# Kernel optimization log

Measured on AMD Instinct MI355X. Metric: run time of the kernel, lower is better.

The kernel has to match this reference:

```python
import jax, jax.numpy as jnp
import numpy as np


def silu(x):
    return x * jax.nn.sigmoid(x)


def setup_inputs() -> dict:
    key = jax.random.key(0)
    ks = jax.random.split(key, 12)
    B, S, Dm = 2, 2048, 768
    I, N, R, K = 1536, 16, 48, 4
    s = 0.02
    return {
        "input_states": jax.random.normal(ks[0], (B, S, Dm), jnp.float32),
        "in_proj_w": jax.random.normal(ks[1], (2 * I, Dm), jnp.float32) * s,
        "conv_w": jax.random.normal(ks[2], (I, 1, K), jnp.float32) * s,
        "conv_b": jax.random.normal(ks[3], (I,), jnp.float32) * s,
        "x_proj_w": jax.random.normal(ks[4], (R + 2 * N, I), jnp.float32) * s,
        "dt_proj_w": jax.random.normal(ks[5], (I, R), jnp.float32) * s,
        "dt_proj_b": jax.random.normal(ks[6], (I,), jnp.float32) * s,
        "A_log": jax.random.normal(ks[7], (I, N), jnp.float32) * 0.5,
        "D": jax.random.normal(ks[8], (I,), jnp.float32) * s,
        "out_proj_w": jax.random.normal(ks[9], (Dm, I), jnp.float32) * s,
        "alpha": jax.random.uniform(ks[10], (I,), jnp.float32),
        "feature_gating": jax.random.uniform(ks[11], (I,), jnp.float32),
    }


def reference(input_states, in_proj_w, conv_w, conv_b, x_proj_w,
              dt_proj_w, dt_proj_b, A_log, D, out_proj_w,
              alpha, feature_gating):
    Bsz, S, _ = input_states.shape
    I, N = A_log.shape
    R = dt_proj_w.shape[1]
    K = conv_w.shape[-1]

    # in_proj (no bias), chunk into hidden / gate, each [B, I, S]
    proj = jnp.einsum('bsd,ed->bse', input_states, in_proj_w)  # [B, S, 2I]
    hidden, gate = jnp.split(proj.transpose(0, 2, 1), 2, axis=1)

    # causal depthwise conv1d + SiLU
    h = jax.lax.conv_general_dilated(
        hidden, conv_w, window_strides=(1,), padding=[(K - 1, 0)],
        dimension_numbers=('NCH', 'OIH', 'NCH'), feature_group_count=I)
    h = silu(h + conv_b[None, :, None])  # [B, I, S]

    # x_proj -> time_step, B, C
    ssm_p = jnp.einsum('bis,ei->bse', h, x_proj_w)  # [B, S, R+2N]
    ts, Bm, Cm = jnp.split(ssm_p, [R, R + N], axis=-1)

    dt = jax.nn.softplus(jnp.einsum('bsr,ir->bsi', ts, dt_proj_w) + dt_proj_b)
    dt = dt.transpose(0, 2, 1)                       # [B, I, S]
    dt = dt.at[:, :, -1].multiply(alpha[None, :])    # alpha scales last step

    A = -jnp.exp(A_log.astype(jnp.float32))          # [I, N]
    dA = jnp.exp(A[None, :, None, :] * dt[:, :, :, None])       # [B, I, S, N]
    dBu = dt[:, :, :, None] * Bm[:, None, :, :] * h[:, :, :, None]  # [B, I, S, N]

    def step(state, xs):
        dA_t, dBu_t, C_t = xs
        state = dA_t * state + dBu_t                 # [B, I, N]
        y = jnp.einsum('bin,bn->bi', state, C_t)
        return state, y

    init = jnp.zeros((Bsz, I, N), input_states.dtype)
    _, ys = jax.lax.scan(
        step, init,
        (dA.transpose(2, 0, 1, 3), dBu.transpose(2, 0, 1, 3), Cm.transpose(1, 0, 2)))
    y = ys.transpose(1, 2, 0)                        # [B, I, S]

    y = (y + h * D[None, :, None]) * silu(gate)
    y = y.at[:, :, -1].multiply(feature_gating[None, :])
    return jnp.einsum('bis,di->bsd', y, out_proj_w)  # [B, S, Dm]
```

## Files before the change

### kernel.cpp

```cpp
#include <hip/hip_runtime.h>
#include <math.h>


static constexpr int S_LEN  = 2048;
static constexpr int DMODEL = 768;
static constexpr int ICH    = 1536;
static constexpr int NST    = 16;
static constexpr int MROWS  = 4096;
static constexpr int NCH    = 64;
static constexpr int CHS    = 32;
static constexpr int CSTR   = 2 * ICH * NST;

typedef _Float16 f16;
typedef f16 f16x8 __attribute__((ext_vector_type(8)));
typedef f16 f16x4 __attribute__((ext_vector_type(4)));
typedef f16 f16x2 __attribute__((ext_vector_type(2)));
typedef float f32x4 __attribute__((ext_vector_type(4)));

typedef __attribute__((address_space(3))) void lds_void;
typedef const __attribute__((address_space(1))) void glb_void;

__device__ __forceinline__ void glds16(f16* l, const f16* g) {
    __builtin_amdgcn_global_load_lds((glb_void*)g, (lds_void*)l, 16, 0, 0);
}

__device__ __forceinline__ float silu_f(float x) {
    return x / (1.0f + __expf(-x));
}

__global__ __launch_bounds__(256) void cvt3(
    const float* __restrict__ s0, f16* __restrict__ d0, int n0,
    const float* __restrict__ s1, f16* __restrict__ d1, int n1,
    const float* __restrict__ s2, f16* __restrict__ d2)
{
    int i = (blockIdx.x * 256 + threadIdx.x) * 4;
    const float* s; f16* d;
    if (i < n0)            { s = s0 + i;            d = d0 + i; }
    else if (i < n0 + n1)  { s = s1 + (i - n0);     d = d1 + (i - n0); }
    else                   { s = s2 + (i - n0 - n1); d = d2 + (i - n0 - n1); }
    float4 v = *(const float4*)s;
    f16x4 o = { (f16)v.x, (f16)v.y, (f16)v.z, (f16)v.w };
    *(f16x4*)d = o;
}

__global__ __launch_bounds__(256) void k1m(
    const f16* __restrict__ Xh,
    const f16* __restrict__ Wh,
    f16* __restrict__ hidden,
    f16* __restrict__ sgate)
{
    __shared__ __align__(16) f16 As[2][128 * 32];
    __shared__ __align__(16) f16 Bs[2][128 * 32];
    const int tid = threadIdx.x;
    const int lane = tid & 63, wave = tid >> 6;
    const int quad = lane >> 4, l16 = lane & 15;
    const int wm = wave & 1, wn = wave >> 1;
    const int m0 = blockIdx.x * 128, n0 = blockIdx.y * 128;
    const int l_row = lane >> 2, l_c8 = (lane & 3) * 8;

    const f16* Ag = Xh + (size_t)(m0 + wave * 16 + l_row) * 768 + l_c8;
    const f16* Bg = Wh + (size_t)(n0 + wave * 16 + l_row) * 768 + l_c8;
    const int lo = (wave * 16) * 32, hi = (64 + wave * 16) * 32;

    f32x4 acc[4][4] = {};
    for (int k0 = 0; k0 < 768; k0 += 64) {
        __syncthreads();
        glds16(&As[0][lo], Ag + k0);
        glds16(&As[0][hi], Ag + (size_t)64 * 768 + k0);
        glds16(&Bs[0][lo], Bg + k0);
        glds16(&Bs[0][hi], Bg + (size_t)64 * 768 + k0);
        glds16(&As[1][lo], Ag + k0 + 32);
        glds16(&As[1][hi], Ag + (size_t)64 * 768 + k0 + 32);
        glds16(&Bs[1][lo], Bg + k0 + 32);
        glds16(&Bs[1][hi], Bg + (size_t)64 * 768 + k0 + 32);
        __syncthreads();
        #pragma unroll
        for (int half = 0; half < 2; ++half) {
            f16x8 af[4], bf[4];
            #pragma unroll
            for (int mi = 0; mi < 4; ++mi)
                af[mi] = *(const f16x8*)&As[half][(wm * 64 + mi * 16 + l16) * 32 + quad * 8];
            #pragma unroll
            for (int ni = 0; ni < 4; ++ni)
                bf[ni] = *(const f16x8*)&Bs[half][(wn * 64 + ni * 16 + l16) * 32 + quad * 8];
            #pragma unroll
            for (int mi = 0; mi < 4; ++mi)
                #pragma unroll
                for (int ni = 0; ni < 4; ++ni)
                    acc[mi][ni] = __builtin_amdgcn_mfma_f32_16x16x32_f16(
                        af[mi], bf[ni], acc[mi][ni], 0, 0, 0);
        }
    }
    const bool isGate = (n0 >= ICH);
    f16* outp = isGate ? sgate : hidden;
    const int e0 = (isGate ? (n0 - ICH) : n0) + wn * 64 + l16;
    #pragma unroll
    for (int mi = 0; mi < 4; ++mi) {
        #pragma unroll
        for (int ni = 0; ni < 4; ++ni) {
            #pragma unroll
            for (int r = 0; r < 4; ++r) {
                int m = m0 + wm * 64 + mi * 16 + quad * 4 + r;
                int e = e0 + ni * 16;
                float v = acc[mi][ni][r];
                if (isGate) v = silu_f(v);
                outp[(size_t)m * ICH + e] = (f16)v;
            }
        }
    }
}

__global__ __launch_bounds__(256) void k2_conv(
    const f16* __restrict__ hidden,
    const float* __restrict__ conv_w,
    const float* __restrict__ conv_b,
    f16* __restrict__ h)
{
    int idx = blockIdx.x * 256 + threadIdx.x;
    int i4 = idx % 384;
    int m  = idx / 384;
    int s  = m & (S_LEN - 1);
    const f16* base = hidden + (size_t)m * ICH + i4 * 4;
    const int c0 = i4 * 4;
    float4 wa = *(const float4*)(conv_w + (c0 + 0) * 4);
    float4 wb = *(const float4*)(conv_w + (c0 + 1) * 4);
    float4 wc = *(const float4*)(conv_w + (c0 + 2) * 4);
    float4 wd = *(const float4*)(conv_w + (c0 + 3) * 4);
    float4 bv = *(const float4*)(conv_b + c0);
    f16x4 z = {};
    f16x4 x0 = *(const f16x4*)(base);
    f16x4 x1 = (s >= 1) ? *(const f16x4*)(base - ICH)     : z;
    f16x4 x2 = (s >= 2) ? *(const f16x4*)(base - 2 * ICH) : z;
    f16x4 x3 = (s >= 3) ? *(const f16x4*)(base - 3 * ICH) : z;
    float r0 = bv.x + wa.x * (float)x3[0] + wa.y * (float)x2[0] + wa.z * (float)x1[0] + wa.w * (float)x0[0];
    float r1 = bv.y + wb.x * (float)x3[1] + wb.y * (float)x2[1] + wb.z * (float)x1[1] + wb.w * (float)x0[1];
    float r2 = bv.z + wc.x * (float)x3[2] + wc.y * (float)x2[2] + wc.z * (float)x1[2] + wc.w * (float)x0[2];
    float r3 = bv.w + wd.x * (float)x3[3] + wd.y * (float)x2[3] + wd.z * (float)x1[3] + wd.w * (float)x0[3];
    f16x4 r = { (f16)silu_f(r0), (f16)silu_f(r1), (f16)silu_f(r2), (f16)silu_f(r3) };
    *(f16x4*)(h + (size_t)m * ICH + i4 * 4) = r;
}

__global__ __launch_bounds__(256) void k3_xproj(
    const f16* __restrict__ h,
    const float* __restrict__ xw,
    float* __restrict__ ssmp)
{
    __shared__ float4 As[64][5];
    __shared__ float4 Bs[80][5];
    const int tid = threadIdx.x;
    const int tm = tid >> 4;
    const int te = tid & 15;
    const int m0 = blockIdx.x * 64;
    const int k_beg = blockIdx.y * 384;
    const int lrow = tid >> 2, lc4 = tid & 3;
    float4 acc[4][5] = {};
    for (int k0 = k_beg; k0 < k_beg + 384; k0 += 16) {
        f16x4 hv = *(const f16x4*)(h + (size_t)(m0 + lrow) * ICH + k0 + lc4 * 4);
        As[lrow][lc4] = make_float4((float)hv[0], (float)hv[1], (float)hv[2], (float)hv[3]);
        for (int t = tid; t < 320; t += 256)
            Bs[t >> 2][t & 3] = *(const float4*)(xw + (size_t)(t >> 2) * ICH + k0 + (t & 3) * 4);
        __syncthreads();
        #pragma unroll
        for (int kk4 = 0; kk4 < 4; ++kk4) {
            float4 a[4], b[5];
            #pragma unroll
            for (int i = 0; i < 4; ++i) a[i] = As[tm + 16 * i][kk4];
            #pragma unroll
            for (int j = 0; j < 5; ++j) b[j] = Bs[te + 16 * j][kk4];
            #pragma unroll
            for (int i = 0; i < 4; ++i)
                #pragma unroll
                for (int j = 0; j < 5; ++j) {
                    acc[i][j].x += a[i].x * b[j].x; acc[i][j].y += a[i].y * b[j].y;
                    acc[i][j].z += a[i].z * b[j].z; acc[i][j].w += a[i].w * b[j].w;
                }
        }
        __syncthreads();
    }
    #pragma unroll
    for (int i = 0; i < 4; ++i) {
        int m = m0 + tm + 16 * i;
        #pragma unroll
        for (int j = 0; j < 5; ++j) {
            float v = acc[i][j].x + acc[i][j].y + acc[i][j].z + acc[i][j].w;
            atomicAdd(ssmp + (size_t)m * 80 + te + 16 * j, v);
        }
    }
}

__global__ __launch_bounds__(256) void k4m(
    const float* __restrict__ ssmp,
    const float* __restrict__ dtw,
    const float* __restrict__ dtb,
    const float* __restrict__ alpha,
    float* __restrict__ dt)
{
    __shared__ __align__(16) f16 As[128 * 72];
    __shared__ __align__(16) f16 Bs[128 * 72];
    const int tid = threadIdx.x;
    const int lane = tid & 63, wave = tid >> 6;
    const int quad = lane >> 4, l16 = lane & 15;
    const int wm = wave & 1, wn = wave >> 1;
    const int m0 = blockIdx.x * 128, n0 = blockIdx.y * 128;
    const int srow = tid >> 1;
    const int shalf = tid & 1;

    {
        const float* sa = ssmp + (size_t)(m0 + srow) * 80 + shalf * 24;
        const float* sb = dtw + (size_t)(n0 + srow) * 48 + shalf * 24;
        f16* da = &As[srow * 72 + shalf * 24];
        f16* db = &Bs[srow * 72 + shalf * 24];
        #pragma unroll
        for (int j = 0; j < 6; ++j) {
            float4 va = *(const float4*)(sa + 4 * j);
            float4 vb = *(const float4*)(sb + 4 * j);
            f16x4 oa = { (f16)va.x, (f16)va.y, (f16)va.z, (f16)va.w };
            f16x4 ob = { (f16)vb.x, (f16)vb.y, (f16)vb.z, (f16)vb.w };
            *(f16x4*)(da + 4 * j) = oa;
            *(f16x4*)(db + 4 * j) = ob;
        }
        if (shalf) {
            f16x8 z = {};
            *(f16x8*)&As[srow * 72 + 48] = z;
            *(f16x8*)&As[srow * 72 + 56] = z;
            *(f16x8*)&Bs[srow * 72 + 48] = z;
            *(f16x8*)&Bs[srow * 72 + 56] = z;
        }
    }
    __syncthreads();

    f32x4 acc[4][4] = {};
    #pragma unroll
    for (int ks = 0; ks < 2; ++ks) {
        f16x8 af[4], bf[4];
        #pragma unroll
        for (int mi = 0; mi < 4; ++mi)
            af[mi] = *(const f16x8*)&As[(wm * 64 + mi * 16 + l16) * 72 + ks * 32 + quad * 8];
        #pragma unroll
        for (int ni = 0; ni < 4; ++ni)
            bf[ni] = *(const f16x8*)&Bs[(wn * 64 + ni * 16 + l16) * 72 + ks * 32 + quad * 8];
        #pragma unroll
        for (int mi = 0; mi < 4; ++mi)
            #pragma unroll
            for (int ni = 0; ni < 4; ++ni)
                acc[mi][ni] = __builtin_amdgcn_mfma_f32_16x16x32_f16(
                    af[mi], bf[ni], acc[mi][ni], 0, 0, 0);
    }

    #pragma unroll
    for (int ni = 0; ni < 4; ++ni) {
        int e = n0 + wn * 64 + ni * 16 + l16;
        float bias = dtb[e];
        float al = alpha[e];
        #pragma unroll
        for (int mi = 0; mi < 4; ++mi) {
            #pragma unroll
            for (int r = 0; r < 4; ++r) {
                int m = m0 + wm * 64 + mi * 16 + quad * 4 + r;
                float x = acc[mi][ni][r] + bias;
                float sp = (x > 20.0f) ? x : __logf(1.0f + __expf(x));
                if ((m & (S_LEN - 1)) == S_LEN - 1) sp *= al;
                dt[(size_t)m * ICH + e] = sp;
            }
        }
    }
}

__global__ __launch_bounds__(256) void k5a_chunk(
    const float* __restrict__ dt,
    const f16* __restrict__ h,
    const float* __restrict__ ssmp,
    const float* __restrict__ A_log,
    float* __restrict__ PArr,
    float* __restrict__ SfArr)
{
    __shared__ float dts[CHS * 64];
    __shared__ float hs[CHS * 64];
    __shared__ float Bc[CHS][16];
    const int tid = threadIdx.x;
    const int n4 = tid & 3;
    const int il = tid >> 2;
    const int i0 = blockIdx.x * 64;
    const int i = i0 + il;
    const int c = blockIdx.y;
    const int b = blockIdx.z;
    const int s0 = c * CHS;
    const size_t row0 = (size_t)(b * S_LEN + s0) * ICH + i0;

    #pragma unroll
    for (int k = 0; k < (CHS * 64) / 256; ++k) {
        int idx = tid + k * 256;
        dts[idx] = dt[row0 + (size_t)(idx >> 6) * ICH + (idx & 63)];
    }
    #pragma unroll
    for (int k = 0; k < (CHS * 64) / 512; ++k) {
        int idx = (tid + k * 256) * 2;
        f16x2 v = *(const f16x2*)(h + row0 + (size_t)(idx >> 6) * ICH + (idx & 63));
        hs[idx] = (float)v[0]; hs[idx + 1] = (float)v[1];
    }
    if (tid < CHS * 4) {
        int t = tid >> 2, q = tid & 3;
        *(float4*)&Bc[t][q * 4] =
            *(const float4*)(ssmp + (size_t)(b * S_LEN + s0 + t) * 80 + 48 + q * 4);
    }

    const float L2E = 1.44269504088896f;
    float4 alv = *(const float4*)(A_log + i * NST + n4 * 4);
    float A[4] = { -expf(alv.x) * L2E, -expf(alv.y) * L2E,
                   -expf(alv.z) * L2E, -expf(alv.w) * L2E };
    float st[4] = {};
    float cdt = 0.f;
    __syncthreads();
    #pragma unroll 4
    for (int t = 0; t < CHS; ++t) {
        float dtv = dts[t * 64 + il];
        float hv  = hs[t * 64 + il];
        float4 Bv = *(const float4*)&Bc[t][n4 * 4];
        cdt += dtv;
        float x = dtv * hv;
        #pragma unroll
        for (int j = 0; j < 4; ++j) {
            float dA = exp2f(A[j] * dtv);
            st[j] = fmaf(dA, st[j], x * (&Bv.x)[j]);
        }
    }
    size_t base = (size_t)c * CSTR + (size_t)(b * ICH + i) * NST + n4 * 4;
    float4 Pv = { exp2f(A[0] * cdt), exp2f(A[1] * cdt),
                  exp2f(A[2] * cdt), exp2f(A[3] * cdt) };
    float4 Sv = { st[0], st[1], st[2], st[3] };
    *(float4*)(PArr + base)  = Pv;
    *(float4*)(SfArr + base) = Sv;
}

__global__ __launch_bounds__(256) void k5b_carry(
    const float* PArr,
    const float* __restrict__ SfArr,
    float* CIn)
{
    int idx = blockIdx.x * 256 + threadIdx.x;
    float carry = 0.f;
    #pragma unroll 8
    for (int c = 0; c < NCH; ++c) {
        size_t a = (size_t)c * CSTR + idx;
        float p = PArr[a];
        float s = SfArr[a];
        CIn[a] = carry;
        carry = fmaf(p, carry, s);
    }
}

__global__ __launch_bounds__(256) void k5c_emit(
    const float* __restrict__ dt,
    const f16* __restrict__ h,
    const f16* __restrict__ sgate,
    const float* __restrict__ ssmp,
    const float* __restrict__ A_log,
    const float* __restrict__ Dp,
    const float* __restrict__ fg,
    const float* __restrict__ CIn,
    f16* __restrict__ yh)
{
    __shared__ float dts[CHS * 64];
    __shared__ float hs[CHS * 64];
    __shared__ float gs[CHS * 64];
    __shared__ float BC[CHS][32];
    const int tid = threadIdx.x;
    const int n4 = tid & 3;
    const int il = tid >> 2;
    const int i0 = blockIdx.x * 64;
    const int i = i0 + il;
    const int c = blockIdx.y;
    const int b = blockIdx.z;
    const int s0 = c * CHS;
    const size_t row0 = (size_t)(b * S_LEN + s0) * ICH + i0;

    #pragma unroll
    for (int k = 0; k < (CHS * 64) / 256; ++k) {
        int idx = tid + k * 256;
        dts[idx] = dt[row0 + (size_t)(idx >> 6) * ICH + (idx & 63)];
    }
    #pragma unroll
    for (int k = 0; k < (CHS * 64) / 512; ++k) {
        int idx = (tid + k * 256) * 2;
        size_t g_off = row0 + (size_t)(idx >> 6) * ICH + (idx & 63);
        f16x2 v = *(const f16x2*)(h + g_off);
        f16x2 w = *(const f16x2*)(sgate + g_off);
        hs[idx] = (float)v[0]; hs[idx + 1] = (float)v[1];
        gs[idx] = (float)w[0]; gs[idx + 1] = (float)w[1];
    }
    {
        int t = tid >> 3, q = tid & 7;
        *(float4*)&BC[t][q * 4] =
            *(const float4*)(ssmp + (size_t)(b * S_LEN + s0 + t) * 80 + 48 + q * 4);
    }

    const float L2E = 1.44269504088896f;
    float4 alv = *(const float4*)(A_log + i * NST + n4 * 4);
    float A[4] = { -expf(alv.x) * L2E, -expf(alv.y) * L2E,
                   -expf(alv.z) * L2E, -expf(alv.w) * L2E };
    const float Dv = Dp[i];
    const float fgv = fg[i];
    float4 civ = *(const float4*)(CIn + (size_t)c * CSTR + (size_t)(b * ICH + i) * NST + n4 * 4);
    float st[4] = { civ.x, civ.y, civ.z, civ.w };
    f16* yout = yh + row0 + il;
    const bool last_chunk = (c == NCH - 1);
    __syncthreads();
    #pragma unroll 4
    for (int t = 0; t < CHS; ++t) {
        float dtv = dts[t * 64 + il];
        float hv  = hs[t * 64 + il];
        float4 Bv = *(const float4*)&BC[t][n4 * 4];
        float4 Cv = *(const float4*)&BC[t][16 + n4 * 4];
        float x = dtv * hv;
        float yp = 0.f;
        #pragma unroll
        for (int j = 0; j < 4; ++j) {
            float dA = exp2f(A[j] * dtv);
            st[j] = fmaf(dA, st[j], x * (&Bv.x)[j]);
            yp = fmaf(st[j], (&Cv.x)[j], yp);
        }
        yp += __shfl_xor(yp, 1, 4);
        yp += __shfl_xor(yp, 2, 4);
        if (n4 == 0) {
            float yv = fmaf(hv, Dv, yp) * gs[t * 64 + il];
            if (last_chunk && t == CHS - 1) yv *= fgv;
            yout[(size_t)t * ICH] = (f16)yv;
        }
    }
}

__global__ __launch_bounds__(256) void k6m(
    const f16* __restrict__ Yh,
    const f16* __restrict__ Wh,
    float* __restrict__ out)
{
    __shared__ __align__(16) f16 As[2][128 * 32];
    __shared__ __align__(16) f16 Bs[2][128 * 32];
    const int tid = threadIdx.x;
    const int lane = tid & 63, wave = tid >> 6;
    const int quad = lane >> 4, l16 = lane & 15;
    const int wm = wave & 1, wn = wave >> 1;
    const int m0 = blockIdx.x * 128, n0 = blockIdx.y * 128;
    const int l_row = lane >> 2, l_c8 = (lane & 3) * 8;

    const f16* Ag = Yh + (size_t)(m0 + wave * 16 + l_row) * ICH + l_c8;
    const f16* Bg = Wh + (size_t)(n0 + wave * 16 + l_row) * ICH + l_c8;
    const int lo = (wave * 16) * 32, hi = (64 + wave * 16) * 32;

    f32x4 acc[4][4] = {};
    for (int k0 = 0; k0 < ICH; k0 += 64) {
        __syncthreads();
        glds16(&As[0][lo], Ag + k0);
        glds16(&As[0][hi], Ag + (size_t)64 * ICH + k0);
        glds16(&Bs[0][lo], Bg + k0);
        glds16(&Bs[0][hi], Bg + (size_t)64 * ICH + k0);
        glds16(&As[1][lo], Ag + k0 + 32);
        glds16(&As[1][hi], Ag + (size_t)64 * ICH + k0 + 32);
        glds16(&Bs[1][lo], Bg + k0 + 32);
        glds16(&Bs[1][hi], Bg + (size_t)64 * ICH + k0 + 32);
        __syncthreads();
        #pragma unroll
        for (int half = 0; half < 2; ++half) {
            f16x8 af[4], bf[4];
            #pragma unroll
            for (int mi = 0; mi < 4; ++mi)
                af[mi] = *(const f16x8*)&As[half][(wm * 64 + mi * 16 + l16) * 32 + quad * 8];
            #pragma unroll
            for (int ni = 0; ni < 4; ++ni)
                bf[ni] = *(const f16x8*)&Bs[half][(wn * 64 + ni * 16 + l16) * 32 + quad * 8];
            #pragma unroll
            for (int mi = 0; mi < 4; ++mi)
                #pragma unroll
                for (int ni = 0; ni < 4; ++ni)
                    acc[mi][ni] = __builtin_amdgcn_mfma_f32_16x16x32_f16(
                        af[mi], bf[ni], acc[mi][ni], 0, 0, 0);
        }
    }
    #pragma unroll
    for (int mi = 0; mi < 4; ++mi) {
        #pragma unroll
        for (int ni = 0; ni < 4; ++ni) {
            #pragma unroll
            for (int r = 0; r < 4; ++r) {
                int m = m0 + wm * 64 + mi * 16 + quad * 4 + r;
                int d = n0 + wn * 64 + ni * 16 + l16;
                out[(size_t)m * DMODEL + d] = acc[mi][ni][r];
            }
        }
    }
}

extern "C" void kernel_launch(void* const* d_in, const int* in_sizes, int n_in,
                              void* d_out, int out_size, void* d_ws, size_t ws_size,
                              hipStream_t stream) {
    const float* X     = (const float*)d_in[0];
    const float* W1    = (const float*)d_in[1];
    const float* CW    = (const float*)d_in[2];
    const float* CB    = (const float*)d_in[3];
    const float* XW    = (const float*)d_in[4];
    const float* DTW   = (const float*)d_in[5];
    const float* DTB   = (const float*)d_in[6];
    const float* ALOG  = (const float*)d_in[7];
    const float* DD    = (const float*)d_in[8];
    const float* OW    = (const float*)d_in[9];
    const float* ALPHA = (const float*)d_in[10];
    const float* FG    = (const float*)d_in[11];
    float* out = (float*)d_out;

    const size_t NBI = (size_t)MROWS * ICH;
    f16* hidden_h = (f16*)d_ws;
    f16* sgate_h  = hidden_h + NBI;
    f16* h_h      = sgate_h + NBI;
    float* dtbuf  = (float*)(h_h + NBI);
    float* ssmp   = dtbuf + NBI;
    f16* Xh       = (f16*)(ssmp + (size_t)MROWS * 80);
    f16* W1h      = Xh + (size_t)MROWS * DMODEL;
    f16* OWh      = W1h + (size_t)2 * ICH * DMODEL;
    float* SfA    = (float*)(OWh + (size_t)DMODEL * ICH);
    float* PArr = (float*)hidden_h;
    float* CIn  = PArr;
    f16* yh     = (f16*)SfA;

    const int nX = MROWS * DMODEL, nW1 = 2 * ICH * DMODEL, nOW = DMODEL * ICH;
    hipMemsetAsync(ssmp, 0, (size_t)MROWS * 80 * sizeof(float), stream);
    cvt3<<<dim3((nX + nW1 + nOW) / 1024), 256, 0, stream>>>(X, Xh, nX, W1, W1h, nW1, OW, OWh);
    k1m<<<dim3(32, 24), 256, 0, stream>>>(Xh, W1h, hidden_h, sgate_h);
    k2_conv<<<dim3((MROWS * 384) / 256), 256, 0, stream>>>(hidden_h, CW, CB, h_h);
    k3_xproj<<<dim3(64, 4), 256, 0, stream>>>(h_h, XW, ssmp);
    k4m<<<dim3(32, 12), 256, 0, stream>>>(ssmp, DTW, DTB, ALPHA, dtbuf);
    k5a_chunk<<<dim3(24, NCH, 2), 256, 0, stream>>>(dtbuf, h_h, ssmp, ALOG, PArr, SfA);
    k5b_carry<<<dim3(192), 256, 0, stream>>>(PArr, SfA, CIn);
    k5c_emit<<<dim3(24, NCH, 2), 256, 0, stream>>>(dtbuf, h_h, sgate_h, ssmp, ALOG, DD, FG, CIn, yh);
    k6m<<<dim3(32, 6), 256, 0, stream>>>(yh, OWh, out);
}
```

Before: 297.5 us.

## Move x_proj to MFMA fp16 and store dt buffer as fp16

Replaces the scalar FP32 x_proj GEMM with an MFMA 16x16x32 f16 kernel that uses 128-row tiles, a 192-wide K split and global_load_lds for the activation tile. Separately, the dt buffer written by the dt projection and read twice by the scan kernels is stored in half precision, halving that traffic. Both changes lower precision: x_proj weights are converted to fp16 per tile, and dt is rounded to fp16 before the exponentials in the scan, which can introduce error.

```diff
diff --git a/kernel.cpp b/kernel.cpp
--- a/kernel.cpp
+++ b/kernel.cpp
@@ -140,50 +140,61 @@
     *(f16x4*)(h + (size_t)m * ICH + i4 * 4) = r;
 }
 
-__global__ __launch_bounds__(256) void k3_xproj(
+__global__ __launch_bounds__(256) void k3m(
     const f16* __restrict__ h,
     const float* __restrict__ xw,
     float* __restrict__ ssmp)
 {
-    __shared__ float4 As[64][5];
-    __shared__ float4 Bs[80][5];
+    __shared__ __align__(16) f16 Ah[128 * 32];
+    __shared__ __align__(16) f16 Bh[80 * 32];
     const int tid = threadIdx.x;
-    const int tm = tid >> 4;
-    const int te = tid & 15;
-    const int m0 = blockIdx.x * 64;
-    const int k_beg = blockIdx.y * 384;
-    const int lrow = tid >> 2, lc4 = tid & 3;
-    float4 acc[4][5] = {};
-    for (int k0 = k_beg; k0 < k_beg + 384; k0 += 16) {
-        f16x4 hv = *(const f16x4*)(h + (size_t)(m0 + lrow) * ICH + k0 + lc4 * 4);
-        As[lrow][lc4] = make_float4((float)hv[0], (float)hv[1], (float)hv[2], (float)hv[3]);
-        for (int t = tid; t < 320; t += 256)
-            Bs[t >> 2][t & 3] = *(const float4*)(xw + (size_t)(t >> 2) * ICH + k0 + (t & 3) * 4);
+    const int lane = tid & 63, wave = tid >> 6;
+    const int quad = lane >> 4, l16 = lane & 15;
+    const int m0 = blockIdx.x * 128;
+    const int kbeg = blockIdx.y * 192;
+    const int l_row = lane >> 2, l_c8 = (lane & 3) * 8;
+
+    const f16* Ag = h + (size_t)(m0 + wave * 32 + l_row) * ICH + l_c8;
+    f16* As0 = Ah + (wave * 32) * 32;
+    f16* As1 = Ah + (wave * 32 + 16) * 32;
+
+    f32x4 acc[2][5] = {};
+    for (int k0 = kbeg; k0 < kbeg + 192; k0 += 32) {
         __syncthreads();
-        #pragma unroll
-        for (int kk4 = 0; kk4 < 4; ++kk4) {
-            float4 a[4], b[5];
-            #pragma unroll
-            for (int i = 0; i < 4; ++i) a[i] = As[tm + 16 * i][kk4];
-            #pragma unroll
-            for (int j = 0; j < 5; ++j) b[j] = Bs[te + 16 * j][kk4];
-            #pragma unroll
-            for (int i = 0; i < 4; ++i)
-                #pragma unroll
-                for (int j = 0; j < 5; ++j) {
-                    acc[i][j].x += a[i].x * b[j].x; acc[i][j].y += a[i].y * b[j].y;
-                    acc[i][j].z += a[i].z * b[j].z; acc[i][j].w += a[i].w * b[j].w;
-                }
+        glds16(As0, Ag + k0);
+        glds16(As1, Ag + (size_t)16 * ICH + k0);
+        {
+            int c4 = (tid & 7) * 4;
+            for (int r = tid >> 3; r < 80; r += 32) {
+                float4 v = *(const float4*)(xw + (size_t)r * ICH + k0 + c4);
+                f16x4 o = { (f16)v.x, (f16)v.y, (f16)v.z, (f16)v.w };
+                *(f16x4*)&Bh[r * 32 + c4] = o;
+            }
         }
         __syncthreads();
-    }
-    #pragma unroll
-    for (int i = 0; i < 4; ++i) {
-        int m = m0 + tm + 16 * i;
+        f16x8 af[2], bf[5];
+        #pragma unroll
+        for (int mi = 0; mi < 2; ++mi)
+            af[mi] = *(const f16x8*)&Ah[(wave * 32 + mi * 16 + l16) * 32 + quad * 8];
+        #pragma unroll
+        for (int j = 0; j < 5; ++j)
+            bf[j] = *(const f16x8*)&Bh[(j * 16 + l16) * 32 + quad * 8];
+        #pragma unroll
+        for (int mi = 0; mi < 2; ++mi)
+            #pragma unroll
+            for (int j = 0; j < 5; ++j)
+                acc[mi][j] = __builtin_amdgcn_mfma_f32_16x16x32_f16(
+                    af[mi], bf[j], acc[mi][j], 0, 0, 0);
+    }
+    #pragma unroll
+    for (int mi = 0; mi < 2; ++mi) {
         #pragma unroll
         for (int j = 0; j < 5; ++j) {
-            float v = acc[i][j].x + acc[i][j].y + acc[i][j].z + acc[i][j].w;
-            atomicAdd(ssmp + (size_t)m * 80 + te + 16 * j, v);
+            #pragma unroll
+            for (int r = 0; r < 4; ++r) {
+                int m = m0 + wave * 32 + mi * 16 + quad * 4 + r;
+                atomicAdd(ssmp + (size_t)m * 80 + j * 16 + l16, acc[mi][j][r]);
+            }
         }
     }
 }
@@ -193,7 +204,7 @@
     const float* __restrict__ dtw,
     const float* __restrict__ dtb,
     const float* __restrict__ alpha,
-    float* __restrict__ dt)
+    f16* __restrict__ dt)
 {
     __shared__ __align__(16) f16 As[128 * 72];
     __shared__ __align__(16) f16 Bs[128 * 72];
@@ -260,14 +271,14 @@
                 float x = acc[mi][ni][r] + bias;
                 float sp = (x > 20.0f) ? x : __logf(1.0f + __expf(x));
                 if ((m & (S_LEN - 1)) == S_LEN - 1) sp *= al;
-                dt[(size_t)m * ICH + e] = sp;
+                dt[(size_t)m * ICH + e] = (f16)sp;
             }
         }
     }
 }
 
 __global__ __launch_bounds__(256) void k5a_chunk(
-    const float* __restrict__ dt,
+    const f16* __restrict__ dt,
     const f16* __restrict__ h,
     const float* __restrict__ ssmp,
     const float* __restrict__ A_log,
@@ -288,15 +299,13 @@
     const size_t row0 = (size_t)(b * S_LEN + s0) * ICH + i0;
 
     #pragma unroll
-    for (int k = 0; k < (CHS * 64) / 256; ++k) {
-        int idx = tid + k * 256;
-        dts[idx] = dt[row0 + (size_t)(idx >> 6) * ICH + (idx & 63)];
-    }
-    #pragma unroll
     for (int k = 0; k < (CHS * 64) / 512; ++k) {
         int idx = (tid + k * 256) * 2;
-        f16x2 v = *(const f16x2*)(h + row0 + (size_t)(idx >> 6) * ICH + (idx & 63));
-        hs[idx] = (float)v[0]; hs[idx + 1] = (float)v[1];
+        size_t g_off = row0 + (size_t)(idx >> 6) * ICH + (idx & 63);
+        f16x2 dv = *(const f16x2*)(dt + g_off);
+        f16x2 hv = *(const f16x2*)(h + g_off);
+        dts[idx] = (float)dv[0]; dts[idx + 1] = (float)dv[1];
+        hs[idx]  = (float)hv[0]; hs[idx + 1]  = (float)hv[1];
     }
     if (tid < CHS * 4) {
         int t = tid >> 2, q = tid & 3;
@@ -350,7 +359,7 @@
 }
 
 __global__ __launch_bounds__(256) void k5c_emit(
-    const float* __restrict__ dt,
+    const f16* __restrict__ dt,
     const f16* __restrict__ h,
     const f16* __restrict__ sgate,
     const float* __restrict__ ssmp,
@@ -375,16 +384,13 @@
     const size_t row0 = (size_t)(b * S_LEN + s0) * ICH + i0;
 
     #pragma unroll
-    for (int k = 0; k < (CHS * 64) / 256; ++k) {
-        int idx = tid + k * 256;
-        dts[idx] = dt[row0 + (size_t)(idx >> 6) * ICH + (idx & 63)];
-    }
-    #pragma unroll
     for (int k = 0; k < (CHS * 64) / 512; ++k) {
         int idx = (tid + k * 256) * 2;
         size_t g_off = row0 + (size_t)(idx >> 6) * ICH + (idx & 63);
+        f16x2 dv = *(const f16x2*)(dt + g_off);
         f16x2 v = *(const f16x2*)(h + g_off);
         f16x2 w = *(const f16x2*)(sgate + g_off);
+        dts[idx] = (float)dv[0]; dts[idx + 1] = (float)dv[1];
         hs[idx] = (float)v[0]; hs[idx + 1] = (float)v[1];
         gs[idx] = (float)w[0]; gs[idx + 1] = (float)w[1];
     }
@@ -511,8 +517,8 @@
     f16* hidden_h = (f16*)d_ws;
     f16* sgate_h  = hidden_h + NBI;
     f16* h_h      = sgate_h + NBI;
-    float* dtbuf  = (float*)(h_h + NBI);
-    float* ssmp   = dtbuf + NBI;
+    f16* dt_h     = h_h + NBI;
+    float* ssmp   = (float*)(dt_h + NBI);
     f16* Xh       = (f16*)(ssmp + (size_t)MROWS * 80);
     f16* W1h      = Xh + (size_t)MROWS * DMODEL;
     f16* OWh      = W1h + (size_t)2 * ICH * DMODEL;
@@ -526,10 +532,10 @@
     cvt3<<<dim3((nX + nW1 + nOW) / 1024), 256, 0, stream>>>(X, Xh, nX, W1, W1h, nW1, OW, OWh);
     k1m<<<dim3(32, 24), 256, 0, stream>>>(Xh, W1h, hidden_h, sgate_h);
     k2_conv<<<dim3((MROWS * 384) / 256), 256, 0, stream>>>(hidden_h, CW, CB, h_h);
-    k3_xproj<<<dim3(64, 4), 256, 0, stream>>>(h_h, XW, ssmp);
-    k4m<<<dim3(32, 12), 256, 0, stream>>>(ssmp, DTW, DTB, ALPHA, dtbuf);
-    k5a_chunk<<<dim3(24, NCH, 2), 256, 0, stream>>>(dtbuf, h_h, ssmp, ALOG, PArr, SfA);
+    k3m<<<dim3(32, 8), 256, 0, stream>>>(h_h, XW, ssmp);
+    k4m<<<dim3(32, 12), 256, 0, stream>>>(ssmp, DTW, DTB, ALPHA, dt_h);
+    k5a_chunk<<<dim3(24, NCH, 2), 256, 0, stream>>>(dt_h, h_h, ssmp, ALOG, PArr, SfA);
     k5b_carry<<<dim3(192), 256, 0, stream>>>(PArr, SfA, CIn);
-    k5c_emit<<<dim3(24, NCH, 2), 256, 0, stream>>>(dtbuf, h_h, sgate_h, ssmp, ALOG, DD, FG, CIn, yh);
+    k5c_emit<<<dim3(24, NCH, 2), 256, 0, stream>>>(dt_h, h_h, sgate_h, ssmp, ALOG, DD, FG, CIn, yh);
     k6m<<<dim3(32, 6), 256, 0, stream>>>(yh, OWh, out);
 }
```

Result: faster. 279.7 us (-6.0%).
